# Optimization experiments

Measured on AMD Instinct MI355X. Metric: run time of the kernel, lower is better.

## Reference

```python
import jax, jax.numpy as jnp
import numpy as np

T, B, A, I, H, L = 256, 64, 512, 1024, 1024, 2
STDV = 1.0 / np.sqrt(H)

def _uniform(key, shape):
    return jax.random.uniform(key, shape, jnp.float32, -STDV, STDV)

def setup_inputs() -> dict:
    key = jax.random.key(0)
    ks = jax.random.split(key, 11)
    return {
        "attention": jax.random.normal(ks[0], (T, B, A), jnp.float32),
        "x": jax.random.normal(ks[1], (T, B, I), jnp.float32),
        "ping": jax.random.normal(ks[2], (B,), jnp.float32),  # unused by module
        "h0": jax.random.normal(ks[3], (L, B, H), jnp.float32),
        "c0": jax.random.normal(ks[4], (L, B, H), jnp.float32),
        "weight_ah": _uniform(ks[5], (L, A, 4 * H)),
        "weight_ih": _uniform(ks[6], (L, I, 4 * H)),  # input_size == hidden_size so layers stack
        "weight_hh": _uniform(ks[7], (L, H, 4 * H)),
        "bias_ah": _uniform(ks[8], (L, 4 * H)),
        "bias_ih": _uniform(ks[9], (L, 4 * H)),
        "bias_hh": _uniform(ks[10], (L, 4 * H)),
    }

def reference(attention, x, ping, h0, c0, weight_ah, weight_ih, weight_hh, bias_ah, bias_ih, bias_hh):
    # Faithful to SACILSTM.forward: only attention[0] is used (fixed across t),
    # ping is unused; per layer l, state is initialized from init_states[l].
    a0 = attention[0]  # [B, A]
    inputs = x  # [T, B, I]
    h_lasts, c_lasts = [], []
    for l in range(h0.shape[0]):
        w_hh = weight_hh[l]
        # Precompute the time-invariant + input-dependent part of the gates.
        const = a0 @ weight_ah[l] + bias_ah[l] + bias_ih[l] + bias_hh[l]  # [B, 4H]
        xg = jnp.einsum('tbi,ij->tbj', inputs, weight_ih[l]) + const  # [T, B, 4H]

        def step(carry, xg_t):
            h, c = carry
            gates = xg_t + h @ w_hh
            i_g, f_g, g_g, o_g = jnp.split(gates, 4, axis=-1)
            c = jax.nn.sigmoid(f_g) * c + jax.nn.sigmoid(i_g) * jnp.tanh(g_g)
            h = jax.nn.sigmoid(o_g) * jnp.tanh(c)
            return (h, c), h

        (h_T, c_T), hs = jax.lax.scan(step, (h0[l], c0[l]), xg)
        inputs = hs  # [T, B, H] feeds next layer
        h_lasts.append(h_T)
        c_lasts.append(c_T)
    # (self.h[:, -1], (self.h[-1], self.c[-1])) flattened
    return hs, jnp.stack(h_lasts), jnp.stack(c_lasts)
```

## Files before the change

### kernel.cpp

```cpp
#include <hip/hip_runtime.h>
#include <hip/hip_bf16.h>
#include <stdint.h>

#define TT 256
#define BB 64
#define AA 512
#define II 1024
#define HH 1024
#define LL 2
#define BH 65536
#define B4H 262144
#define OUT_HL 16777216
#define OUT_CL (16777216 + 131072)
#define NBLK 256

typedef __attribute__((ext_vector_type(8))) short bf16x8;
typedef __attribute__((ext_vector_type(4))) float f32x4;
typedef __attribute__((ext_vector_type(4))) unsigned int u32x4;
typedef __attribute__((ext_vector_type(2))) unsigned int u32x2;

__device__ __forceinline__ ushort f2bf(float v) {
    union { float f; uint32_t u; } x; x.f = v;
    uint32_t r = x.u + 0x7fff + ((x.u >> 16) & 1);
    return (ushort)(r >> 16);
}

__device__ __forceinline__ float sigf(float x) {
    return 1.f / (1.f + __expf(-x));
}


__global__ __launch_bounds__(256) void k_prep_wt(const float* __restrict__ wih,
                                                 const float* __restrict__ whh,
                                                 ushort* __restrict__ Wt) {
    __shared__ ushort tile[64][65];
    const int l = blockIdx.z;
    const int k0 = blockIdx.x * 64;
    const int col0 = blockIdx.y * 64;
    const int tid = threadIdx.x;
    const int cl = tid & 63, ks = tid >> 6;
    const float* src;
    int krow0;
    if (k0 < 1024) { src = wih + (size_t)l * 1024 * 4096; krow0 = k0; }
    else           { src = whh + (size_t)l * 1024 * 4096; krow0 = k0 - 1024; }
#pragma unroll
    for (int i = 0; i < 16; ++i) {
        int kl = ks + i * 4;
        tile[kl][cl] = f2bf(src[(size_t)(krow0 + kl) * 4096 + col0 + cl]);
    }
    __syncthreads();
    const int g0 = col0 >> 10, ub = col0 & 1023;
    ushort* dst = Wt + (size_t)l * 4096 * 2048;
    const int klane = tid & 63;
#pragma unroll
    for (int i = 0; i < 16; ++i) {
        int cl2 = (tid >> 6) + i * 4;
        int row = (ub + cl2) * 4 + g0;
        ushort* p = dst + (size_t)row * 2048 + k0 + klane;
        uint v = (uint)tile[klane][cl2];
        asm volatile("global_store_short %0, %1, off sc0 sc1"
                     :: "v"(p), "v"(v) : "memory");
    }
}

__global__ __launch_bounds__(256) void k_cast_x(const float* __restrict__ x,
                                                ushort* __restrict__ xbfF) {
    int i = blockIdx.x * 256 + threadIdx.x;
    int k8 = i & 127, b = (i >> 7) & 63, t = i >> 13;
    const float4* xs = (const float4*)(x + (((size_t)t * 64 + b) * 1024 + k8 * 8));
    float4 a = xs[0], c = xs[1];
    uint4 pk;
    pk.x = (uint)f2bf(a.x) | ((uint)f2bf(a.y) << 16);
    pk.y = (uint)f2bf(a.z) | ((uint)f2bf(a.w) << 16);
    pk.z = (uint)f2bf(c.x) | ((uint)f2bf(c.y) << 16);
    pk.w = (uint)f2bf(c.z) | ((uint)f2bf(c.w) << 16);
    size_t off = (size_t)t * 65536 + (size_t)(b >> 4) * 16384 +
                 (size_t)(k8 >> 2) * 512 + (size_t)(k8 & 3) * 128 + (size_t)(b & 15) * 8;
    *(uint4*)(xbfF + off) = pk;
}

__global__ __launch_bounds__(256) void k_const(const float* __restrict__ attn,
                                               const float* __restrict__ wah,
                                               const float* __restrict__ bah,
                                               const float* __restrict__ bih,
                                               const float* __restrict__ bhh,
                                               float* __restrict__ constg) {
    const int tid = threadIdx.x;
    const int col = blockIdx.x * 256 + tid;
    const int b0 = blockIdx.y * 8;
    const int l = blockIdx.z;
    const float* W = wah + (size_t)l * 512 * 4096;
    float acc[8] = {0.f, 0.f, 0.f, 0.f, 0.f, 0.f, 0.f, 0.f};
    for (int k = 0; k < 512; ++k) {
        float wv = W[(size_t)k * 4096 + col];
#pragma unroll
        for (int j = 0; j < 8; ++j) acc[j] += attn[(b0 + j) * 512 + k] * wv;
    }
    float bias = bah[l * 4096 + col] + bih[l * 4096 + col] + bhh[l * 4096 + col];
    float* cg = constg + (size_t)l * B4H;
#pragma unroll
    for (int j = 0; j < 8; ++j) cg[(size_t)(b0 + j) * 4096 + col] = acc[j] + bias;
}

__global__ __launch_bounds__(256) void k_init(const float* __restrict__ h0,
                                              ushort* __restrict__ hs0F,
                                              ushort* __restrict__ h1s0,
                                              unsigned* __restrict__ flags) {
    int i = blockIdx.x * 256 + threadIdx.x;
    if (i < 16384) {
        int k8 = i & 127, b = (i >> 7) & 63, l = i >> 13;
        const float* src = h0 + ((size_t)(l * 64 + b) * 1024 + k8 * 8);
        uint4 pk;
        pk.x = (uint)f2bf(src[0]) | ((uint)f2bf(src[1]) << 16);
        pk.y = (uint)f2bf(src[2]) | ((uint)f2bf(src[3]) << 16);
        pk.z = (uint)f2bf(src[4]) | ((uint)f2bf(src[5]) << 16);
        pk.w = (uint)f2bf(src[6]) | ((uint)f2bf(src[7]) << 16);
        size_t off = (size_t)(b >> 4) * 16384 + (size_t)(k8 >> 2) * 512 +
                     (size_t)(k8 & 3) * 128 + (size_t)(b & 15) * 8;
        *(uint4*)((l == 0 ? hs0F : h1s0) + off) = pk;
    }
    if (i < NBLK) flags[i] = 0u;
}

#define ISSUE(BUF, BASE)                                                       \
    do {                                                                       \
        _Pragma("unroll")                                                      \
        for (int _i = 0; _i < 8; ++_i)                                         \
            asm volatile("global_load_dwordx4 %0, %1, off"                     \
                         : "=v"(BUF[_i]) : "v"((BASE) + _i * 512));            \
    } while (0)

#define CONSUME(BUF, c, N)                                                     \
    do {                                                                       \
        asm volatile("s_waitcnt vmcnt(" #N ")" ::: "memory");                  \
        __builtin_amdgcn_sched_barrier(0x100);                                 \
        _Pragma("unroll")                                                      \
        for (int _i = 0; _i < 8; ++_i) {                                       \
            bf16x8 b = *(const bf16x8*)(bbase + ((c) * 8 + _i) * 512);         \
            acc = __builtin_amdgcn_mfma_f32_16x16x32_bf16(BUF[_i], b, acc, 0, 0, 0); \
        }                                                                      \
    } while (0)

__global__ __launch_bounds__(512, 1) void k_persist(
        const ushort* __restrict__ xbfF,
        ushort* __restrict__ hs0F,
        const ushort* __restrict__ h1s0,
        ushort* Wt,
        const float* __restrict__ constg,
        const float* __restrict__ c0,
        float* __restrict__ out,
        unsigned* __restrict__ flags) {
    __shared__ ushort wlds[65536];
    __shared__ float gt[8][16][17];

    const int tid = threadIdx.x;
    const int w = tid >> 6, lane = tid & 63;
    const int layer = w >> 2, wm = w & 3;
    const int u0 = blockIdx.x * 4;
    const int bid = blockIdx.x;

    {
        bf16x8 vst[16];
#pragma unroll
        for (int i = 0; i < 16; ++i) {
            int c = i * 512 + tid;
            int ly = c >> 12, r = c & 4095;
            int col = r >> 8, kg = r & 255;
            const ushort* src = Wt + ((size_t)(ly * 4096 + u0 * 4 + col)) * 2048 + kg * 8;
            asm volatile("global_load_dwordx4 %0, %1, off sc0 sc1"
                         : "=v"(vst[i]) : "v"(src));
        }
        asm volatile("s_waitcnt vmcnt(0)" ::: "memory");
        __builtin_amdgcn_sched_barrier(0);
#pragma unroll
        for (int i = 0; i < 16; ++i) {
            int c = i * 512 + tid;
            int ly = c >> 12, r = c & 4095;
            int col = r >> 8, kg = r & 255;
            int slot = ly * 4096 + kg * 16 + col;
            *(bf16x8*)(wlds + (size_t)slot * 8) = vst[i];
        }
    }

    const int cc = lane & 15;
    const int gu = u0 + (cc >> 2), gg_ = cc & 3, gcol = (gg_ << 10) + gu;
    const int r0 = (lane >> 4) * 4;
    const float* cgp = constg + (size_t)layer * B4H;
    float cg[4];
#pragma unroll
    for (int r = 0; r < 4; ++r)
        cg[r] = cgp[(size_t)(wm * 16 + r0 + r) * 4096 + gcol];

    const int bl = lane & 15, ul = lane >> 4;
    const int eidx = (wm * 16 + bl) * 1024 + (u0 + ul);
    float creg = c0[layer * BH + eidx];

    const size_t fro = (size_t)wm * 16384 + (size_t)lane * 8;
    const int hoff = wm * 16384 + ((u0 >> 5) << 9) + (((u0 >> 3) & 3) << 7) +
                     (bl << 3) + (u0 & 4);
    const ushort* bbase = wlds + ((size_t)layer * 4096 + lane) * 8;

    __syncthreads();

    for (int s = 0; s <= TT; ++s) {
        const int act0 = (layer == 0) && (s < TT);
        const int act1 = (layer == 1) && (s >= 1);
        const int t1 = s - 1;

        bf16x8 bufA[8], bufB[8], bufC[8], bufD[8];

        if (act0) {
            const ushort* Axl = xbfF + (size_t)s * 65536 + fro;
            ISSUE(bufA, Axl + 0 * 4096);
            ISSUE(bufB, Axl + 1 * 4096);
            ISSUE(bufC, Axl + 2 * 4096);
            ISSUE(bufD, Axl + 3 * 4096);
            asm volatile("s_waitcnt vmcnt(0)" ::: "memory");
            __builtin_amdgcn_sched_barrier(0);
        }

        if (s > 0) {
            if (w == 0) {
                const unsigned target = (unsigned)s;
                const unsigned* fp = flags + lane * 4;
                while (true) {
                    u32x4 f;
                    asm volatile("global_load_dwordx4 %0, %1, off sc0 sc1\n\t"
                                 "s_waitcnt vmcnt(0)"
                                 : "=v"(f) : "v"(fp) : "memory");
                    int ok = (f.x >= target) && (f.y >= target) &&
                             (f.z >= target) && (f.w >= target);
                    if (__all(ok)) break;
                    __builtin_amdgcn_s_sleep(2);
                }
            }
            __syncthreads();
        }

        float hv = 0.f, cn = 0.f;
        if (act0 | act1) {
            f32x4 acc = {0.f, 0.f, 0.f, 0.f};
            const ushort* Ahl;
            if (layer == 0) {
                Ahl = hs0F + (size_t)s * 65536 + fro;
            } else {
                const ushort* Axl = hs0F + (size_t)s * 65536 + fro;
                Ahl = (t1 == 0 ? h1s0 : (const ushort*)Wt + (size_t)(t1 - 1) * 65536) + fro;
                ISSUE(bufA, Axl + 0 * 4096);
                ISSUE(bufB, Axl + 1 * 4096);
                ISSUE(bufC, Axl + 2 * 4096);
                ISSUE(bufD, Axl + 3 * 4096);
            }
            CONSUME(bufA, 0, 24); ISSUE(bufA, Ahl + 0 * 4096);
            CONSUME(bufB, 1, 24); ISSUE(bufB, Ahl + 1 * 4096);
            CONSUME(bufC, 2, 24); ISSUE(bufC, Ahl + 2 * 4096);
            CONSUME(bufD, 3, 24); ISSUE(bufD, Ahl + 3 * 4096);
            CONSUME(bufA, 4, 24);
            CONSUME(bufB, 5, 16);
            CONSUME(bufC, 6, 8);
            CONSUME(bufD, 7, 0);
#pragma unroll
            for (int r = 0; r < 4; ++r)
                gt[w][r0 + r][cc] = acc[r] + cg[r];
            __builtin_amdgcn_wave_barrier();
            asm volatile("s_waitcnt lgkmcnt(0)" ::: "memory");
            float gi = gt[w][bl][ul * 4 + 0];
            float gf = gt[w][bl][ul * 4 + 1];
            float gv = gt[w][bl][ul * 4 + 2];
            float go = gt[w][bl][ul * 4 + 3];
            float si = sigf(gi), sf = sigf(gf), so = sigf(go);
            cn = sf * creg + si * (2.f * sigf(2.f * gv) - 1.f);
            hv = so * (2.f * sigf(2.f * cn) - 1.f);
            creg = cn;
            uint hb = (uint)f2bf(hv);
            uint g0 = __shfl(hb, bl);
            uint g1 = __shfl(hb, bl + 16);
            uint g2 = __shfl(hb, bl + 32);
            uint g3 = __shfl(hb, bl + 48);
            u32x2 hp;
            hp.x = (g0 & 0xffffu) | (g1 << 16);
            hp.y = (g2 & 0xffffu) | (g3 << 16);
            ushort* hdst = (layer == 0 ? hs0F + (size_t)(s + 1) * 65536
                                       : Wt + (size_t)t1 * 65536) + hoff;
            if (lane < 16)
                asm volatile("global_store_dwordx2 %0, %1, off sc0 sc1"
                             :: "v"(hdst), "v"(hp) : "memory");
        }

        if (s < TT) {
            asm volatile("s_waitcnt vmcnt(0)" ::: "memory");
            __syncthreads();
            if (tid == 0) {
                unsigned tgt = (unsigned)(s + 1);
                unsigned* fp = flags + bid;
                asm volatile("global_store_dword %0, %1, off sc0 sc1"
                             :: "v"(fp), "v"(tgt) : "memory");
            }
        }

        if (act1) {
            float4 ov;
            ov.x = __shfl(hv, bl);
            ov.y = __shfl(hv, bl + 16);
            ov.z = __shfl(hv, bl + 32);
            ov.w = __shfl(hv, bl + 48);
            if (lane < 16)
                *(float4*)(out + (size_t)t1 * 65536 + (wm * 16 + bl) * 1024 + u0) = ov;
            if (t1 == TT - 1) {
                out[OUT_HL + BH + eidx] = hv;
                out[OUT_CL + BH + eidx] = cn;
            }
        } else if (act0 && s == TT - 1) {
            out[OUT_HL + eidx] = hv;
            out[OUT_CL + eidx] = cn;
        }
    }
}

extern "C" void kernel_launch(void* const* d_in, const int* in_sizes, int n_in,
                              void* d_out, int out_size, void* d_ws, size_t ws_size,
                              hipStream_t stream) {
    const float* attn = (const float*)d_in[0];
    const float* x    = (const float*)d_in[1];
    const float* h0   = (const float*)d_in[3];
    const float* c0   = (const float*)d_in[4];
    const float* wah  = (const float*)d_in[5];
    const float* wih  = (const float*)d_in[6];
    const float* whh  = (const float*)d_in[7];
    const float* bah  = (const float*)d_in[8];
    const float* bih  = (const float*)d_in[9];
    const float* bhh  = (const float*)d_in[10];
    float* out = (float*)d_out;

    char* ws = (char*)d_ws;
    ushort*   Wt     = (ushort*)(ws);
    ushort*   xbfF   = (ushort*)(ws + 33554432);
    ushort*   hs0F   = (ushort*)(ws + 67108864);
    ushort*   h1s0   = (ushort*)(ws + 100794368);
    float*    constg = (float*)(ws + 100925440);
    unsigned* flags  = (unsigned*)(ws + 103022592);

    hipLaunchKernelGGL(k_prep_wt, dim3(32, 64, 2), dim3(256), 0, stream, wih, whh, Wt);
    hipLaunchKernelGGL(k_cast_x, dim3(8192), dim3(256), 0, stream, x, xbfF);
    hipLaunchKernelGGL(k_const, dim3(16, 8, 2), dim3(256), 0, stream, attn, wah, bah, bih, bhh, constg);
    hipLaunchKernelGGL(k_init, dim3(64), dim3(256), 0, stream, h0, hs0F, h1s0, flags);

    void* args[] = { (void*)&xbfF, (void*)&hs0F, (void*)&h1s0, (void*)&Wt,
                     (void*)&constg, (void*)&c0, (void*)&out, (void*)&flags };
    hipLaunchCooperativeKernel((void*)k_persist, dim3(NBLK), dim3(512), args, 0, stream);
}
```

Measured before the change: 1.721 ms.

## Split layers across separate blocks with K-split waves and per-layer flags

Restructures the persistent LSTM kernel so each block handles one layer and 8 hidden units, instead of both layers for 4 units. The two wave groups split the K dimension: one handles the input projection and the other the recurrent projection, and their partial sums are combined through LDS. Each layer polls only the flags it depends on, so layer 0 no longer waits for a global barrier that includes layer 1. The intent is to pipeline the layers and shorten the per-step critical path, at the cost of an extra __syncthreads and LDS reduction per step and a change of launch bounds to 2 blocks per CU.

Measured after the change: 2.074 ms. 1.2x slower.

```diff
diff --git a/kernel.cpp b/kernel.cpp
--- a/kernel.cpp
+++ b/kernel.cpp
@@ -130,18 +130,34 @@
                          : "=v"(BUF[_i]) : "v"((BASE) + _i * 512));            \
     } while (0)
 
-#define CONSUME(BUF, c, N)                                                     \
+#define CONSUME2(BUF, c, N)                                                    \
     do {                                                                       \
         asm volatile("s_waitcnt vmcnt(" #N ")" ::: "memory");                  \
         __builtin_amdgcn_sched_barrier(0x100);                                 \
         _Pragma("unroll")                                                      \
         for (int _i = 0; _i < 8; ++_i) {                                       \
-            bf16x8 b = *(const bf16x8*)(bbase + ((c) * 8 + _i) * 512);         \
-            acc = __builtin_amdgcn_mfma_f32_16x16x32_bf16(BUF[_i], b, acc, 0, 0, 0); \
+            int _ktg = kh * 32 + (c) * 8 + _i;                                 \
+            bf16x8 _b0 = *(const bf16x8*)(wlds + (size_t)_ktg * 1024 + lane * 8);       \
+            bf16x8 _b1 = *(const bf16x8*)(wlds + (size_t)_ktg * 1024 + 512 + lane * 8); \
+            acc0 = __builtin_amdgcn_mfma_f32_16x16x32_bf16(BUF[_i], _b0, acc0, 0, 0, 0);\
+            acc1 = __builtin_amdgcn_mfma_f32_16x16x32_bf16(BUF[_i], _b1, acc1, 0, 0, 0);\
         }                                                                      \
     } while (0)
 
-__global__ __launch_bounds__(512, 1) void k_persist(
+#define POLL(FB, TGT)                                                          \
+    do {                                                                       \
+        const unsigned* _fp = (FB) + lane * 2;                                 \
+        while (true) {                                                         \
+            u32x2 _f;                                                          \
+            asm volatile("global_load_dwordx2 %0, %1, off sc0 sc1\n\t"         \
+                         "s_waitcnt vmcnt(0)"                                  \
+                         : "=v"(_f) : "v"(_fp) : "memory");                    \
+            if (__all(_f.x >= (TGT) && _f.y >= (TGT))) break;                  \
+            __builtin_amdgcn_s_sleep(2);                                       \
+        }                                                                      \
+    } while (0)
+
+__global__ __launch_bounds__(512, 2) void k_persist(
         const ushort* __restrict__ xbfF,
         ushort* __restrict__ hs0F,
         const ushort* __restrict__ h1s0,
@@ -151,22 +167,24 @@
         float* __restrict__ out,
         unsigned* __restrict__ flags) {
     __shared__ ushort wlds[65536];
-    __shared__ float gt[8][16][17];
+    __shared__ float gt[2][4][2][16][17];
 
     const int tid = threadIdx.x;
     const int w = tid >> 6, lane = tid & 63;
-    const int layer = w >> 2, wm = w & 3;
-    const int u0 = blockIdx.x * 4;
+    const int kh = w >> 2, m = w & 3;
     const int bid = blockIdx.x;
+    const int layer = bid >> 7, ub = bid & 127;
+    const int u0g = ub * 8;
 
     {
         bf16x8 vst[16];
 #pragma unroll
         for (int i = 0; i < 16; ++i) {
             int c = i * 512 + tid;
-            int ly = c >> 12, r = c & 4095;
-            int col = r >> 8, kg = r & 255;
-            const ushort* src = Wt + ((size_t)(ly * 4096 + u0 * 4 + col)) * 2048 + kg * 8;
+            int lp = c & 63, nt = (c >> 6) & 1, ktg = c >> 7;
+            int colp = u0g * 4 + nt * 16 + (lp & 15);
+            int kk = ktg * 32 + (lp >> 4) * 8;
+            const ushort* src = Wt + ((size_t)(layer * 4096 + colp)) * 2048 + kk;
             asm volatile("global_load_dwordx4 %0, %1, off sc0 sc1"
                          : "=v"(vst[i]) : "v"(src));
         }
@@ -175,144 +193,142 @@
 #pragma unroll
         for (int i = 0; i < 16; ++i) {
             int c = i * 512 + tid;
-            int ly = c >> 12, r = c & 4095;
-            int col = r >> 8, kg = r & 255;
-            int slot = ly * 4096 + kg * 16 + col;
-            *(bf16x8*)(wlds + (size_t)slot * 8) = vst[i];
-        }
-    }
-
-    const int cc = lane & 15;
-    const int gu = u0 + (cc >> 2), gg_ = cc & 3, gcol = (gg_ << 10) + gu;
-    const int r0 = (lane >> 4) * 4;
-    const float* cgp = constg + (size_t)layer * B4H;
-    float cg[4];
-#pragma unroll
-    for (int r = 0; r < 4; ++r)
-        cg[r] = cgp[(size_t)(wm * 16 + r0 + r) * 4096 + gcol];
-
-    const int bl = lane & 15, ul = lane >> 4;
-    const int eidx = (wm * 16 + bl) * 1024 + (u0 + ul);
-    float creg = c0[layer * BH + eidx];
-
-    const size_t fro = (size_t)wm * 16384 + (size_t)lane * 8;
-    const int hoff = wm * 16384 + ((u0 >> 5) << 9) + (((u0 >> 3) & 3) << 7) +
-                     (bl << 3) + (u0 & 4);
-    const ushort* bbase = wlds + ((size_t)layer * 4096 + lane) * 8;
+            *(bf16x8*)(wlds + (size_t)c * 8) = vst[i];
+        }
+    }
+
+    const int bl = lane & 15, ud = lane >> 4;
+
+    float cgA[4], cgB[4], cA = 0.f, cB = 0.f;
+    if (kh == 0) {
+        const float* cgp = constg + (size_t)layer * B4H +
+                           (size_t)(m * 16 + bl) * 4096 + u0g + ud;
+#pragma unroll
+        for (int g = 0; g < 4; ++g) { cgA[g] = cgp[g * 1024]; cgB[g] = cgp[g * 1024 + 4]; }
+        cA = c0[layer * BH + (m * 16 + bl) * 1024 + u0g + ud];
+        cB = c0[layer * BH + (m * 16 + bl) * 1024 + u0g + ud + 4];
+    }
+
+    const size_t fro = (size_t)m * 16384 + (size_t)lane * 8;
+    const int hoff = m * 16384 + (ub >> 2) * 512 + (ub & 3) * 128 + bl * 8;
+    const unsigned* f0 = flags;
+    const unsigned* f1 = flags + 128;
 
     __syncthreads();
 
-    for (int s = 0; s <= TT; ++s) {
-        const int act0 = (layer == 0) && (s < TT);
-        const int act1 = (layer == 1) && (s >= 1);
+    const int sBeg = layer ? 1 : 0;
+    const int sEnd = layer ? TT : (TT - 1);
+    for (int s = sBeg; s <= sEnd; ++s) {
         const int t1 = s - 1;
-
         bf16x8 bufA[8], bufB[8], bufC[8], bufD[8];
-
-        if (act0) {
-            const ushort* Axl = xbfF + (size_t)s * 65536 + fro;
-            ISSUE(bufA, Axl + 0 * 4096);
-            ISSUE(bufB, Axl + 1 * 4096);
-            ISSUE(bufC, Axl + 2 * 4096);
-            ISSUE(bufD, Axl + 3 * 4096);
-            asm volatile("s_waitcnt vmcnt(0)" ::: "memory");
-            __builtin_amdgcn_sched_barrier(0);
-        }
-
-        if (s > 0) {
-            if (w == 0) {
-                const unsigned target = (unsigned)s;
-                const unsigned* fp = flags + lane * 4;
-                while (true) {
-                    u32x4 f;
-                    asm volatile("global_load_dwordx4 %0, %1, off sc0 sc1\n\t"
-                                 "s_waitcnt vmcnt(0)"
-                                 : "=v"(f) : "v"(fp) : "memory");
-                    int ok = (f.x >= target) && (f.y >= target) &&
-                             (f.z >= target) && (f.w >= target);
-                    if (__all(ok)) break;
-                    __builtin_amdgcn_s_sleep(2);
-                }
-            }
-            __syncthreads();
-        }
-
-        float hv = 0.f, cn = 0.f;
-        if (act0 | act1) {
-            f32x4 acc = {0.f, 0.f, 0.f, 0.f};
-            const ushort* Ahl;
+        f32x4 acc0 = {0.f, 0.f, 0.f, 0.f}, acc1 = {0.f, 0.f, 0.f, 0.f};
+
+        if (kh == 0) {
+            const ushort* Al;
             if (layer == 0) {
-                Ahl = hs0F + (size_t)s * 65536 + fro;
+                Al = xbfF + (size_t)s * 65536 + fro;
             } else {
-                const ushort* Axl = hs0F + (size_t)s * 65536 + fro;
-                Ahl = (t1 == 0 ? h1s0 : (const ushort*)Wt + (size_t)(t1 - 1) * 65536) + fro;
-                ISSUE(bufA, Axl + 0 * 4096);
-                ISSUE(bufB, Axl + 1 * 4096);
-                ISSUE(bufC, Axl + 2 * 4096);
-                ISSUE(bufD, Axl + 3 * 4096);
-            }
-            CONSUME(bufA, 0, 24); ISSUE(bufA, Ahl + 0 * 4096);
-            CONSUME(bufB, 1, 24); ISSUE(bufB, Ahl + 1 * 4096);
-            CONSUME(bufC, 2, 24); ISSUE(bufC, Ahl + 2 * 4096);
-            CONSUME(bufD, 3, 24); ISSUE(bufD, Ahl + 3 * 4096);
-            CONSUME(bufA, 4, 24);
-            CONSUME(bufB, 5, 16);
-            CONSUME(bufC, 6, 8);
-            CONSUME(bufD, 7, 0);
-#pragma unroll
-            for (int r = 0; r < 4; ++r)
-                gt[w][r0 + r][cc] = acc[r] + cg[r];
-            __builtin_amdgcn_wave_barrier();
-            asm volatile("s_waitcnt lgkmcnt(0)" ::: "memory");
-            float gi = gt[w][bl][ul * 4 + 0];
-            float gf = gt[w][bl][ul * 4 + 1];
-            float gv = gt[w][bl][ul * 4 + 2];
-            float go = gt[w][bl][ul * 4 + 3];
-            float si = sigf(gi), sf = sigf(gf), so = sigf(go);
-            cn = sf * creg + si * (2.f * sigf(2.f * gv) - 1.f);
-            hv = so * (2.f * sigf(2.f * cn) - 1.f);
-            creg = cn;
-            uint hb = (uint)f2bf(hv);
-            uint g0 = __shfl(hb, bl);
-            uint g1 = __shfl(hb, bl + 16);
-            uint g2 = __shfl(hb, bl + 32);
-            uint g3 = __shfl(hb, bl + 48);
-            u32x2 hp;
-            hp.x = (g0 & 0xffffu) | (g1 << 16);
-            hp.y = (g2 & 0xffffu) | (g3 << 16);
+                POLL(f0, (unsigned)s);
+                Al = hs0F + (size_t)s * 65536 + fro;
+            }
+            ISSUE(bufA, Al + 0 * 4096);
+            ISSUE(bufB, Al + 1 * 4096);
+            ISSUE(bufC, Al + 2 * 4096);
+            ISSUE(bufD, Al + 3 * 4096);
+        } else {
+            const ushort* Al;
+            if (layer == 0) {
+                if (s >= 1) POLL(f0, (unsigned)s);
+                Al = hs0F + (size_t)s * 65536 + fro;
+            } else {
+                if (t1 >= 1) POLL(f1, (unsigned)s);
+                Al = (t1 == 0 ? h1s0
+                              : (const ushort*)Wt + (size_t)(t1 - 1) * 65536) + fro;
+            }
+            ISSUE(bufA, Al + 0 * 4096);
+            ISSUE(bufB, Al + 1 * 4096);
+            ISSUE(bufC, Al + 2 * 4096);
+            ISSUE(bufD, Al + 3 * 4096);
+        }
+        CONSUME2(bufA, 0, 24);
+        CONSUME2(bufB, 1, 16);
+        CONSUME2(bufC, 2, 8);
+        CONSUME2(bufD, 3, 0);
+
+        {
+            const int r0 = ud * 4;
+#pragma unroll
+            for (int r = 0; r < 4; ++r) {
+                gt[kh][m][0][r0 + r][bl] = acc0[r];
+                gt[kh][m][1][r0 + r][bl] = acc1[r];
+            }
+        }
+        __syncthreads();
+
+        float hvA = 0.f, hvB = 0.f, cnA = 0.f, cnB = 0.f;
+        if (kh == 0) {
+            float gA[4], gB[4];
+#pragma unroll
+            for (int g = 0; g < 4; ++g) {
+                gA[g] = gt[0][m][0][bl][ud * 4 + g] + gt[1][m][0][bl][ud * 4 + g] + cgA[g];
+                gB[g] = gt[0][m][1][bl][ud * 4 + g] + gt[1][m][1][bl][ud * 4 + g] + cgB[g];
+            }
+            float siA = sigf(gA[0]), sfA = sigf(gA[1]), soA = sigf(gA[3]);
+            cnA = sfA * cA + siA * (2.f * sigf(2.f * gA[2]) - 1.f);
+            hvA = soA * (2.f * sigf(2.f * cnA) - 1.f);
+            cA = cnA;
+            float siB = sigf(gB[0]), sfB = sigf(gB[1]), soB = sigf(gB[3]);
+            cnB = sfB * cB + siB * (2.f * sigf(2.f * gB[2]) - 1.f);
+            hvB = soB * (2.f * sigf(2.f * cnB) - 1.f);
+            cB = cnB;
+            uint hbA = (uint)f2bf(hvA), hbB = (uint)f2bf(hvB);
+            uint q0 = __shfl(hbA, bl),      q1 = __shfl(hbA, bl + 16);
+            uint q2 = __shfl(hbA, bl + 32), q3 = __shfl(hbA, bl + 48);
+            uint q4 = __shfl(hbB, bl),      q5 = __shfl(hbB, bl + 16);
+            uint q6 = __shfl(hbB, bl + 32), q7 = __shfl(hbB, bl + 48);
+            u32x4 hp;
+            hp.x = (q0 & 0xffffu) | (q1 << 16);
+            hp.y = (q2 & 0xffffu) | (q3 << 16);
+            hp.z = (q4 & 0xffffu) | (q5 << 16);
+            hp.w = (q6 & 0xffffu) | (q7 << 16);
             ushort* hdst = (layer == 0 ? hs0F + (size_t)(s + 1) * 65536
                                        : Wt + (size_t)t1 * 65536) + hoff;
             if (lane < 16)
-                asm volatile("global_store_dwordx2 %0, %1, off sc0 sc1"
+                asm volatile("global_store_dwordx4 %0, %1, off sc0 sc1"
                              :: "v"(hdst), "v"(hp) : "memory");
         }
 
-        if (s < TT) {
-            asm volatile("s_waitcnt vmcnt(0)" ::: "memory");
-            __syncthreads();
-            if (tid == 0) {
-                unsigned tgt = (unsigned)(s + 1);
-                unsigned* fp = flags + bid;
-                asm volatile("global_store_dword %0, %1, off sc0 sc1"
-                             :: "v"(fp), "v"(tgt) : "memory");
-            }
-        }
-
-        if (act1) {
-            float4 ov;
-            ov.x = __shfl(hv, bl);
-            ov.y = __shfl(hv, bl + 16);
-            ov.z = __shfl(hv, bl + 32);
-            ov.w = __shfl(hv, bl + 48);
-            if (lane < 16)
-                *(float4*)(out + (size_t)t1 * 65536 + (wm * 16 + bl) * 1024 + u0) = ov;
-            if (t1 == TT - 1) {
-                out[OUT_HL + BH + eidx] = hv;
-                out[OUT_CL + BH + eidx] = cn;
-            }
-        } else if (act0 && s == TT - 1) {
-            out[OUT_HL + eidx] = hv;
-            out[OUT_CL + eidx] = cn;
+        asm volatile("s_waitcnt vmcnt(0)" ::: "memory");
+        __syncthreads();
+        if (tid == 0) {
+            unsigned tgt = (unsigned)(s + 1);
+            unsigned* fp = flags + layer * 128 + ub;
+            asm volatile("global_store_dword %0, %1, off sc0 sc1"
+                         :: "v"(fp), "v"(tgt) : "memory");
+        }
+
+        if (kh == 0) {
+            if (layer == 1) {
+                float o0 = __shfl(hvA, bl),      o1 = __shfl(hvA, bl + 16);
+                float o2 = __shfl(hvA, bl + 32), o3 = __shfl(hvA, bl + 48);
+                float o4 = __shfl(hvB, bl),      o5 = __shfl(hvB, bl + 16);
+                float o6 = __shfl(hvB, bl + 32), o7 = __shfl(hvB, bl + 48);
+                if (lane < 16) {
+                    float4 v0 = {o0, o1, o2, o3}, v1 = {o4, o5, o6, o7};
+                    float* op = out + (size_t)t1 * 65536 + (size_t)(m * 16 + bl) * 1024 + u0g;
+                    *(float4*)op = v0;
+                    *(float4*)(op + 4) = v1;
+                }
+                if (t1 == TT - 1) {
+                    int idx = (m * 16 + bl) * 1024 + u0g + ud;
+                    out[OUT_HL + BH + idx] = hvA;  out[OUT_CL + BH + idx] = cnA;
+                    out[OUT_HL + BH + idx + 4] = hvB;  out[OUT_CL + BH + idx + 4] = cnB;
+                }
+            } else if (s == TT - 1) {
+                int idx = (m * 16 + bl) * 1024 + u0g + ud;
+                out[OUT_HL + idx] = hvA;  out[OUT_CL + idx] = cnA;
+                out[OUT_HL + idx + 4] = hvB;  out[OUT_CL + idx + 4] = cnB;
+            }
         }
     }
 }
```
